# Kernel tuning notes

Hardware: AMD Instinct MI355X
Metric: run time of the kernel (lower is better)

The kernel has to match this reference:

```python
import jax, jax.numpy as jnp
import numpy as np

EPS = 1e-8


def setup_inputs() -> dict:
    key = jax.random.key(0)
    k1, k2, k3, k4, k5 = jax.random.split(key, 5)
    B, N_LOG, N_PHYS, E = 16, 512, 2048, 2048
    P = jax.random.uniform(k1, (B, N_LOG, N_PHYS), dtype=jnp.float32)
    d_hw = jax.random.randint(k2, (N_PHYS, N_PHYS), 0, 4, dtype=jnp.int32)
    edge_src = jax.random.randint(k3, (B, E), 0, N_LOG, dtype=jnp.int32)
    edge_dst = jax.random.randint(k4, (B, E), 0, N_LOG, dtype=jnp.int32)
    edge_w = jax.random.uniform(k5, (B, E), dtype=jnp.float32)
    return {"P": P, "d_hw": d_hw, "edge_src": edge_src,
            "edge_dst": edge_dst, "edge_w": edge_w}


def reference(P, d_hw, edge_src, edge_dst, edge_w):
    # A_hw[p,q] = 1 where hardware distance == 1 (adjacent qubits)
    A_hw = (d_hw == 1).astype(P.dtype)                      # [Q, Q]
    B = P.shape[0]
    # Dense contraction once per batch: PA[b,i,q] = sum_p P[b,i,p] A[p,q]
    PA = jnp.einsum('bip,pq->biq', P, A_hw)                 # [B, N, Q]
    b_idx = jnp.arange(B)[:, None]                          # [B, 1]
    gi = PA[b_idx, edge_src]                                # [B, E, Q]
    gj = P[b_idx, edge_dst]                                 # [B, E, Q]
    adj_score = jnp.einsum('beq,beq->be', gi, gj)           # [B, E]
    sample_adj = jnp.sum(edge_w * adj_score, axis=-1)       # [B]
    sample_weight = jnp.maximum(jnp.sum(edge_w, axis=-1), EPS)
    # every sample has edges -> valid_samples = B
    loss = -jnp.mean(sample_adj / sample_weight)
    return loss
```

## Files before the change

### kernel.cpp

```cpp
#include <hip/hip_runtime.h>
#include <hip/hip_bf16.h>

#define BATCH 16
#define NLOG 512
#define Q 2048
#define NEDGE 2048
#define M_TOT (BATCH * NLOG)
#define KB 2048
#define EDOT_BLOCKS 256

typedef float f32x2 __attribute__((ext_vector_type(2)));
typedef float f32x4 __attribute__((ext_vector_type(4)));
typedef int i32x4 __attribute__((ext_vector_type(4)));
typedef int i32x8 __attribute__((ext_vector_type(8)));

__device__ __forceinline__ unsigned char to_e4m3(float f) {
    int pk = __builtin_amdgcn_cvt_pk_fp8_f32(f, f, 0, false);
    return (unsigned char)(pk & 0xff);
}

__device__ __forceinline__ float dot16(i32x4 a, i32x4 b) {
    float s0 = 0.f, s1 = 0.f;
    #pragma unroll
    for (int d = 0; d < 4; d++) {
        f32x2 alo = __builtin_amdgcn_cvt_pk_f32_fp8(a[d], false);
        f32x2 ahi = __builtin_amdgcn_cvt_pk_f32_fp8(a[d], true);
        f32x2 blo = __builtin_amdgcn_cvt_pk_f32_fp8(b[d], false);
        f32x2 bhi = __builtin_amdgcn_cvt_pk_f32_fp8(b[d], true);
        s0 += alo[0] * blo[0] + alo[1] * blo[1];
        s1 += ahi[0] * bhi[0] + ahi[1] * bhi[1];
    }
    return s0 + s1;
}

__global__ __launch_bounds__(256) void prep(const float* __restrict__ P,
                                            unsigned char* __restrict__ P8,
                                            const int* __restrict__ d_hw,
                                            unsigned char* __restrict__ A8t,
                                            float* __restrict__ adj,
                                            float* __restrict__ wsum,
                                            unsigned* __restrict__ counter) {
    int bid = blockIdx.x;
    if (bid == 0) {
        if (threadIdx.x == 0) *counter = 0u;
        if (threadIdx.x < BATCH) { adj[threadIdx.x] = 0.f; wsum[threadIdx.x] = 0.f; }
    }
    if (bid < 8192) {
        int i = (bid * 256 + threadIdx.x) * 8;
        float4 v0 = *(const float4*)(P + i);
        float4 v1 = *(const float4*)(P + i + 4);
        int lo = 0, hi = 0;
        lo = __builtin_amdgcn_cvt_pk_fp8_f32(v0.x, v0.y, lo, false);
        lo = __builtin_amdgcn_cvt_pk_fp8_f32(v0.z, v0.w, lo, true);
        hi = __builtin_amdgcn_cvt_pk_fp8_f32(v1.x, v1.y, hi, false);
        hi = __builtin_amdgcn_cvt_pk_fp8_f32(v1.z, v1.w, hi, true);
        int2 st; st.x = lo; st.y = hi;
        *(int2*)(P8 + i) = st;
    } else {
        bid -= 8192;
        __shared__ unsigned char tile[32][33];
        int q0 = (bid & 63) * 32;
        int p0 = (bid >> 6) * 32;
        int tx = threadIdx.x & 31;
        int ty = threadIdx.x >> 5;
        for (int s = 0; s < 32; s += 8) {
            int p = p0 + ty + s;
            int v = d_hw[(size_t)p * Q + q0 + tx];
            tile[ty + s][tx] = (v == 1) ? 0x38 : 0x00;
        }
        __syncthreads();
        for (int s = 0; s < 32; s += 8) {
            A8t[(size_t)(q0 + ty + s) * Q + p0 + tx] = tile[tx][ty + s];
        }
    }
}

__global__ __launch_bounds__(256, 2) void gemm_bt8(const unsigned char* __restrict__ A,
                                                   const unsigned char* __restrict__ Bt,
                                                   unsigned char* __restrict__ PA8) {
    __shared__ unsigned char As[32768];
    __shared__ unsigned char Bs[16384];

    const int t = threadIdx.x;
    const int w = t >> 6;
    const int wr = w >> 1, wc = w & 1;
    const int l = t & 63;
    const int quad = l >> 4;
    const int lane16 = l & 15;

    const int m0 = blockIdx.x * 256;
    const int n0 = blockIdx.y * 128;

    const int s_row = t >> 3;
    const int s_off = (((t & 7) ^ (s_row & 7)) << 4);

    const int r7 = lane16 & 7;
    const int c0 = ((2 * quad) ^ r7) << 4;
    const int c1 = ((2 * quad + 1) ^ r7) << 4;

    f32x4 acc[8][4] = {};

    for (int k0 = 0; k0 < KB; k0 += 128) {
        #pragma unroll
        for (int c = 0; c < 8; c++) {
            const unsigned char* g = A + (size_t)(m0 + c * 32 + s_row) * KB + k0 + s_off;
            __builtin_amdgcn_global_load_lds(
                (const __attribute__((address_space(1))) void*)g,
                (__attribute__((address_space(3))) void*)(As + c * 4096 + w * 1024),
                16, 0, 0);
        }
        #pragma unroll
        for (int c = 0; c < 4; c++) {
            const unsigned char* g = Bt + (size_t)(n0 + c * 32 + s_row) * KB + k0 + s_off;
            __builtin_amdgcn_global_load_lds(
                (const __attribute__((address_space(1))) void*)g,
                (__attribute__((address_space(3))) void*)(Bs + c * 4096 + w * 1024),
                16, 0, 0);
        }
        __syncthreads();

        i32x8 bfr[4];
        #pragma unroll
        for (int j = 0; j < 4; j++) {
            int base = (wc * 64 + j * 16 + lane16) << 7;
            i32x4 lo = *(const i32x4*)(Bs + base + c0);
            i32x4 hi = *(const i32x4*)(Bs + base + c1);
            bfr[j] = __builtin_shufflevector(lo, hi, 0, 1, 2, 3, 4, 5, 6, 7);
        }
        #pragma unroll
        for (int i = 0; i < 8; i++) {
            int base = (wr * 128 + i * 16 + lane16) << 7;
            i32x4 lo = *(const i32x4*)(As + base + c0);
            i32x4 hi = *(const i32x4*)(As + base + c1);
            i32x8 af = __builtin_shufflevector(lo, hi, 0, 1, 2, 3, 4, 5, 6, 7);
            #pragma unroll
            for (int j = 0; j < 4; j++)
                acc[i][j] = __builtin_amdgcn_mfma_scale_f32_16x16x128_f8f6f4(
                    af, bfr[j], acc[i][j], 0, 0,
                    0, 127,
                    0, 127);
        }
        __syncthreads();
    }

    #pragma unroll
    for (int i = 0; i < 8; i++) {
        #pragma unroll
        for (int j = 0; j < 4; j++) {
            #pragma unroll
            for (int r = 0; r < 4; r++) {
                int row = m0 + wr * 128 + i * 16 + quad * 4 + r;
                int col = n0 + wc * 64 + j * 16 + lane16;
                PA8[(size_t)row * Q + col] = to_e4m3(acc[i][j][r] * (1.0f / 256.0f));
            }
        }
    }
}

__global__ __launch_bounds__(512) void edge_dot(const unsigned char* __restrict__ PA8,
                                                const unsigned char* __restrict__ P8,
                                                const int* __restrict__ esrc,
                                                const int* __restrict__ edst,
                                                const float* __restrict__ ew,
                                                float* __restrict__ adj,
                                                float* __restrict__ wsum,
                                                unsigned* __restrict__ counter,
                                                float* __restrict__ out) {
    const int lid = blockIdx.x;
    const int b = (lid & 7) | ((lid >> 7) << 3);
    const int chunk = (lid >> 3) & 15;
    const int t = threadIdx.x;
    const int w = t >> 6;
    const int lane = t & 63;

    const int e0 = b * NEDGE + chunk * 128 + w * 16;
    const unsigned char* Ab = PA8 + (size_t)b * NLOG * Q;
    const unsigned char* Bb = P8  + (size_t)b * NLOG * Q;
    const int off = lane * 32;

    int src = esrc[e0], dst = edst[e0];
    float wcur = ew[e0];
    const unsigned char* ap = Ab + (size_t)src * Q + off;
    const unsigned char* bp = Bb + (size_t)dst * Q + off;
    i32x4 A0 = *(const i32x4*)ap;
    i32x4 A1 = *(const i32x4*)(ap + 16);
    i32x4 B0 = *(const i32x4*)bp;
    i32x4 B1 = *(const i32x4*)(bp + 16);

    float acc = 0.f;
    float wacc = 0.f;
    #pragma unroll
    for (int e = 0; e < 16; e++) {
        i32x4 nA0 = A0, nA1 = A1, nB0 = B0, nB1 = B1;
        float wnext = 0.f;
        if (e < 15) {
            int ns = esrc[e0 + e + 1], nd = edst[e0 + e + 1];
            wnext = ew[e0 + e + 1];
            const unsigned char* nap = Ab + (size_t)ns * Q + off;
            const unsigned char* nbp = Bb + (size_t)nd * Q + off;
            nA0 = *(const i32x4*)nap;
            nA1 = *(const i32x4*)(nap + 16);
            nB0 = *(const i32x4*)nbp;
            nB1 = *(const i32x4*)(nbp + 16);
        }
        float p = dot16(A0, B0) + dot16(A1, B1);
        acc += wcur * p;
        wacc += wcur;
        A0 = nA0; A1 = nA1; B0 = nB0; B1 = nB1; wcur = wnext;
    }

    #pragma unroll
    for (int o = 32; o > 0; o >>= 1) acc += __shfl_xor(acc, o);

    __shared__ float ra[8], rw[8];
    if (lane == 0) { ra[w] = acc; rw[w] = wacc; }
    __syncthreads();

    if (t == 0) {
        float a = 0.f, ws = 0.f;
        #pragma unroll
        for (int i = 0; i < 8; i++) { a += ra[i]; ws += rw[i]; }
        atomicAdd(&adj[b],  a * 256.0f);
        atomicAdd(&wsum[b], ws);
        __threadfence();
        if (atomicAdd(counter, 1u) == EDOT_BLOCKS - 1) {
            __threadfence();
            float s = 0.f;
            #pragma unroll
            for (int bb = 0; bb < BATCH; bb++) {
                float av = atomicAdd(&adj[bb], 0.0f);
                float wv = atomicAdd(&wsum[bb], 0.0f);
                s += av / fmaxf(wv, 1e-8f);
            }
            out[0] = -s / (float)BATCH;
        }
    }
}

extern "C" void kernel_launch(void* const* d_in, const int* in_sizes, int n_in,
                              void* d_out, int out_size, void* d_ws, size_t ws_size,
                              hipStream_t stream) {
    const float* P    = (const float*)d_in[0];
    const int* d_hw   = (const int*)d_in[1];
    const int* esrc   = (const int*)d_in[2];
    const int* edst   = (const int*)d_in[3];
    const float* ew   = (const float*)d_in[4];
    float* out        = (float*)d_out;

    char* ws = (char*)d_ws;
    unsigned char* P8  = (unsigned char*)ws;
    unsigned char* A8t = (unsigned char*)(ws + 16777216);
    unsigned char* PA8 = (unsigned char*)(ws + 20971520);
    float* adj         = (float*)(ws + 37748736);
    float* wsum        = (float*)(ws + 37748736 + 64);
    unsigned* counter  = (unsigned*)(ws + 37748736 + 128);

    prep<<<8192 + 4096, 256, 0, stream>>>(P, P8, d_hw, A8t, adj, wsum, counter);
    gemm_bt8<<<dim3(M_TOT / 256, Q / 128), 256, 0, stream>>>(P8, A8t, PA8);
    edge_dot<<<EDOT_BLOCKS, 512, 0, stream>>>(PA8, P8, esrc, edst, ew, adj, wsum, counter, out);
}
```

Baseline: 167.5 us.

## Spread edge_dot over more blocks and move final reduction to separate kernel

After: 177.1 us. 1.06x slower.

```diff
diff --git a/kernel.cpp b/kernel.cpp
--- a/kernel.cpp
+++ b/kernel.cpp
@@ -7,7 +7,7 @@
 #define NEDGE 2048
 #define M_TOT (BATCH * NLOG)
 #define KB 2048
-#define EDOT_BLOCKS 256
+#define EDOT_BLOCKS 2048
 
 typedef float f32x2 __attribute__((ext_vector_type(2)));
 typedef float f32x4 __attribute__((ext_vector_type(4)));
@@ -157,84 +157,89 @@
     }
 }
 
-__global__ __launch_bounds__(512) void edge_dot(const unsigned char* __restrict__ PA8,
+__global__ __launch_bounds__(256) void edge_dot(const unsigned char* __restrict__ PA8,
                                                 const unsigned char* __restrict__ P8,
                                                 const int* __restrict__ esrc,
                                                 const int* __restrict__ edst,
                                                 const float* __restrict__ ew,
                                                 float* __restrict__ adj,
-                                                float* __restrict__ wsum,
-                                                unsigned* __restrict__ counter,
-                                                float* __restrict__ out) {
+                                                float* __restrict__ wsum) {
     const int lid = blockIdx.x;
-    const int b = (lid & 7) | ((lid >> 7) << 3);
-    const int chunk = (lid >> 3) & 15;
+    const int idx = lid >> 3;
+    const int b = (lid & 7) | ((idx >> 7) << 3);
+    const int chunk = idx & 127;
     const int t = threadIdx.x;
     const int w = t >> 6;
     const int lane = t & 63;
-
-    const int e0 = b * NEDGE + chunk * 128 + w * 16;
+    const int off = lane * 32;
+
+    const int e0 = b * NEDGE + chunk * 16 + w * 4;
     const unsigned char* Ab = PA8 + (size_t)b * NLOG * Q;
     const unsigned char* Bb = P8  + (size_t)b * NLOG * Q;
-    const int off = lane * 32;
-
-    int src = esrc[e0], dst = edst[e0];
-    float wcur = ew[e0];
-    const unsigned char* ap = Ab + (size_t)src * Q + off;
-    const unsigned char* bp = Bb + (size_t)dst * Q + off;
-    i32x4 A0 = *(const i32x4*)ap;
-    i32x4 A1 = *(const i32x4*)(ap + 16);
-    i32x4 B0 = *(const i32x4*)bp;
-    i32x4 B1 = *(const i32x4*)(bp + 16);
-
-    float acc = 0.f;
-    float wacc = 0.f;
-    #pragma unroll
-    for (int e = 0; e < 16; e++) {
-        i32x4 nA0 = A0, nA1 = A1, nB0 = B0, nB1 = B1;
-        float wnext = 0.f;
-        if (e < 15) {
-            int ns = esrc[e0 + e + 1], nd = edst[e0 + e + 1];
-            wnext = ew[e0 + e + 1];
-            const unsigned char* nap = Ab + (size_t)ns * Q + off;
-            const unsigned char* nbp = Bb + (size_t)nd * Q + off;
-            nA0 = *(const i32x4*)nap;
-            nA1 = *(const i32x4*)(nap + 16);
-            nB0 = *(const i32x4*)nbp;
-            nB1 = *(const i32x4*)(nbp + 16);
-        }
-        float p = dot16(A0, B0) + dot16(A1, B1);
-        acc += wcur * p;
-        wacc += wcur;
-        A0 = nA0; A1 = nA1; B0 = nB0; B1 = nB1; wcur = wnext;
-    }
+
+    int src0 = esrc[e0 + 0], dst0 = edst[e0 + 0];
+    int src1 = esrc[e0 + 1], dst1 = edst[e0 + 1];
+    int src2 = esrc[e0 + 2], dst2 = edst[e0 + 2];
+    int src3 = esrc[e0 + 3], dst3 = edst[e0 + 3];
+    float w0 = ew[e0 + 0], w1 = ew[e0 + 1], w2 = ew[e0 + 2], w3 = ew[e0 + 3];
+
+    const unsigned char* a0 = Ab + (size_t)src0 * Q + off;
+    const unsigned char* b0 = Bb + (size_t)dst0 * Q + off;
+    const unsigned char* a1 = Ab + (size_t)src1 * Q + off;
+    const unsigned char* b1 = Bb + (size_t)dst1 * Q + off;
+    const unsigned char* a2 = Ab + (size_t)src2 * Q + off;
+    const unsigned char* b2 = Bb + (size_t)dst2 * Q + off;
+    const unsigned char* a3 = Ab + (size_t)src3 * Q + off;
+    const unsigned char* b3 = Bb + (size_t)dst3 * Q + off;
+
+    i32x4 A00 = *(const i32x4*)a0;
+    i32x4 A01 = *(const i32x4*)(a0 + 16);
+    i32x4 B00 = *(const i32x4*)b0;
+    i32x4 B01 = *(const i32x4*)(b0 + 16);
+    i32x4 A10 = *(const i32x4*)a1;
+    i32x4 A11 = *(const i32x4*)(a1 + 16);
+    i32x4 B10 = *(const i32x4*)b1;
+    i32x4 B11 = *(const i32x4*)(b1 + 16);
+
+    float acc = w0 * (dot16(A00, B00) + dot16(A01, B01));
+
+    i32x4 A20 = *(const i32x4*)a2;
+    i32x4 A21 = *(const i32x4*)(a2 + 16);
+    i32x4 B20 = *(const i32x4*)b2;
+    i32x4 B21 = *(const i32x4*)(b2 + 16);
+
+    acc += w1 * (dot16(A10, B10) + dot16(A11, B11));
+
+    i32x4 A30 = *(const i32x4*)a3;
+    i32x4 A31 = *(const i32x4*)(a3 + 16);
+    i32x4 B30 = *(const i32x4*)b3;
+    i32x4 B31 = *(const i32x4*)(b3 + 16);
+
+    acc += w2 * (dot16(A20, B20) + dot16(A21, B21));
+    acc += w3 * (dot16(A30, B30) + dot16(A31, B31));
 
     #pragma unroll
     for (int o = 32; o > 0; o >>= 1) acc += __shfl_xor(acc, o);
-
-    __shared__ float ra[8], rw[8];
+    float wacc = w0 + w1 + w2 + w3;
+
+    __shared__ float ra[4], rw[4];
     if (lane == 0) { ra[w] = acc; rw[w] = wacc; }
     __syncthreads();
-
     if (t == 0) {
-        float a = 0.f, ws = 0.f;
-        #pragma unroll
-        for (int i = 0; i < 8; i++) { a += ra[i]; ws += rw[i]; }
-        atomicAdd(&adj[b],  a * 256.0f);
-        atomicAdd(&wsum[b], ws);
-        __threadfence();
-        if (atomicAdd(counter, 1u) == EDOT_BLOCKS - 1) {
-            __threadfence();
-            float s = 0.f;
-            #pragma unroll
-            for (int bb = 0; bb < BATCH; bb++) {
-                float av = atomicAdd(&adj[bb], 0.0f);
-                float wv = atomicAdd(&wsum[bb], 0.0f);
-                s += av / fmaxf(wv, 1e-8f);
-            }
-            out[0] = -s / (float)BATCH;
-        }
-    }
+        atomicAdd(&adj[b],  (ra[0] + ra[1] + ra[2] + ra[3]) * 256.0f);
+        atomicAdd(&wsum[b], rw[0] + rw[1] + rw[2] + rw[3]);
+    }
+}
+
+__global__ __launch_bounds__(64) void finalize(const float* __restrict__ adj,
+                                               const float* __restrict__ wsum,
+                                               float* __restrict__ out) {
+    const int lane = threadIdx.x;
+    float s = 0.f;
+    if (lane < BATCH) s = adj[lane] / fmaxf(wsum[lane], 1e-8f);
+    #pragma unroll
+    for (int o = 8; o > 0; o >>= 1) s += __shfl_xor(s, o);
+    if (lane == 0) out[0] = -s / (float)BATCH;
 }
 
 extern "C" void kernel_launch(void* const* d_in, const int* in_sizes, int n_in,
@@ -257,5 +262,6 @@
 
     prep<<<8192 + 4096, 256, 0, stream>>>(P, P8, d_hw, A8t, adj, wsum, counter);
     gemm_bt8<<<dim3(M_TOT / 256, Q / 128), 256, 0, stream>>>(P8, A8t, PA8);
-    edge_dot<<<EDOT_BLOCKS, 512, 0, stream>>>(PA8, P8, esrc, edst, ew, adj, wsum, counter, out);
-}
+    edge_dot<<<EDOT_BLOCKS, 256, 0, stream>>>(PA8, P8, esrc, edst, ew, adj, wsum);
+    finalize<<<1, 64, 0, stream>>>(adj, wsum, out);
+}
```

## Double-buffer LDS in fp8 GEMM and split tile across 8 waves

Applied to the files above, without the earlier changes.

New measurement: 175.2 us. +4.6%, slower.

```diff
diff --git a/kernel.cpp b/kernel.cpp
--- a/kernel.cpp
+++ b/kernel.cpp
@@ -75,15 +75,60 @@
     }
 }
 
-__global__ __launch_bounds__(256, 2) void gemm_bt8(const unsigned char* __restrict__ A,
+#define GSTAGE(bufAs, bufBs, kk0)                                              \
+    {                                                                          \
+        _Pragma("unroll")                                                      \
+        for (int c = 0; c < 4; c++) {                                          \
+            const unsigned char* g =                                           \
+                A + (size_t)(m0 + c * 64 + s_row) * KB + (kk0) + s_off;        \
+            __builtin_amdgcn_global_load_lds(                                  \
+                (const __attribute__((address_space(1))) void*)g,              \
+                (__attribute__((address_space(3))) void*)((bufAs) + c * 8192 + w * 1024), \
+                16, 0, 0);                                                     \
+        }                                                                      \
+        _Pragma("unroll")                                                      \
+        for (int c = 0; c < 2; c++) {                                          \
+            const unsigned char* g =                                           \
+                Bt + (size_t)(n0 + c * 64 + s_row) * KB + (kk0) + s_off;       \
+            __builtin_amdgcn_global_load_lds(                                  \
+                (const __attribute__((address_space(1))) void*)g,              \
+                (__attribute__((address_space(3))) void*)((bufBs) + c * 8192 + w * 1024), \
+                16, 0, 0);                                                     \
+        }                                                                      \
+    }
+
+#define GCOMPUTE(bufAs, bufBs)                                                 \
+    {                                                                          \
+        i32x8 bfr[2];                                                          \
+        _Pragma("unroll")                                                      \
+        for (int j = 0; j < 2; j++) {                                          \
+            int base = (wc * 32 + j * 16 + lane16) << 7;                       \
+            i32x4 lo = *(const i32x4*)((bufBs) + base + c0);                   \
+            i32x4 hi = *(const i32x4*)((bufBs) + base + c1);                   \
+            bfr[j] = __builtin_shufflevector(lo, hi, 0, 1, 2, 3, 4, 5, 6, 7);  \
+        }                                                                      \
+        _Pragma("unroll")                                                      \
+        for (int i = 0; i < 8; i++) {                                          \
+            int base = (wr * 128 + i * 16 + lane16) << 7;                      \
+            i32x4 lo = *(const i32x4*)((bufAs) + base + c0);                   \
+            i32x4 hi = *(const i32x4*)((bufAs) + base + c1);                   \
+            i32x8 af = __builtin_shufflevector(lo, hi, 0, 1, 2, 3, 4, 5, 6, 7);\
+            _Pragma("unroll")                                                  \
+            for (int j = 0; j < 2; j++)                                        \
+                acc[i][j] = __builtin_amdgcn_mfma_scale_f32_16x16x128_f8f6f4(  \
+                    af, bfr[j], acc[i][j], 0, 0, 0, 127, 0, 127);              \
+        }                                                                      \
+    }
+
+__global__ __launch_bounds__(512, 2) void gemm_bt8(const unsigned char* __restrict__ A,
                                                    const unsigned char* __restrict__ Bt,
                                                    unsigned char* __restrict__ PA8) {
-    __shared__ unsigned char As[32768];
-    __shared__ unsigned char Bs[16384];
+    __shared__ unsigned char As[2][32768];
+    __shared__ unsigned char Bs[2][16384];
 
     const int t = threadIdx.x;
     const int w = t >> 6;
-    const int wr = w >> 1, wc = w & 1;
+    const int wr = w >> 2, wc = w & 3;
     const int l = t & 63;
     const int quad = l >> 4;
     const int lane16 = l & 15;
@@ -98,59 +143,28 @@
     const int c0 = ((2 * quad) ^ r7) << 4;
     const int c1 = ((2 * quad + 1) ^ r7) << 4;
 
-    f32x4 acc[8][4] = {};
-
-    for (int k0 = 0; k0 < KB; k0 += 128) {
-        #pragma unroll
-        for (int c = 0; c < 8; c++) {
-            const unsigned char* g = A + (size_t)(m0 + c * 32 + s_row) * KB + k0 + s_off;
-            __builtin_amdgcn_global_load_lds(
-                (const __attribute__((address_space(1))) void*)g,
-                (__attribute__((address_space(3))) void*)(As + c * 4096 + w * 1024),
-                16, 0, 0);
-        }
-        #pragma unroll
-        for (int c = 0; c < 4; c++) {
-            const unsigned char* g = Bt + (size_t)(n0 + c * 32 + s_row) * KB + k0 + s_off;
-            __builtin_amdgcn_global_load_lds(
-                (const __attribute__((address_space(1))) void*)g,
-                (__attribute__((address_space(3))) void*)(Bs + c * 4096 + w * 1024),
-                16, 0, 0);
-        }
+    f32x4 acc[8][2] = {};
+
+    GSTAGE(As[0], Bs[0], 0);
+    __syncthreads();
+
+    #pragma unroll 2
+    for (int kk = 0; kk < 15; kk++) {
+        const int cur = kk & 1;
+        GSTAGE(As[cur ^ 1], Bs[cur ^ 1], (kk + 1) * 128);
+        GCOMPUTE(As[cur], Bs[cur]);
         __syncthreads();
-
-        i32x8 bfr[4];
-        #pragma unroll
-        for (int j = 0; j < 4; j++) {
-            int base = (wc * 64 + j * 16 + lane16) << 7;
-            i32x4 lo = *(const i32x4*)(Bs + base + c0);
-            i32x4 hi = *(const i32x4*)(Bs + base + c1);
-            bfr[j] = __builtin_shufflevector(lo, hi, 0, 1, 2, 3, 4, 5, 6, 7);
-        }
-        #pragma unroll
-        for (int i = 0; i < 8; i++) {
-            int base = (wr * 128 + i * 16 + lane16) << 7;
-            i32x4 lo = *(const i32x4*)(As + base + c0);
-            i32x4 hi = *(const i32x4*)(As + base + c1);
-            i32x8 af = __builtin_shufflevector(lo, hi, 0, 1, 2, 3, 4, 5, 6, 7);
-            #pragma unroll
-            for (int j = 0; j < 4; j++)
-                acc[i][j] = __builtin_amdgcn_mfma_scale_f32_16x16x128_f8f6f4(
-                    af, bfr[j], acc[i][j], 0, 0,
-                    0, 127,
-                    0, 127);
-        }
-        __syncthreads();
-    }
+    }
+    GCOMPUTE(As[1], Bs[1]);
 
     #pragma unroll
     for (int i = 0; i < 8; i++) {
         #pragma unroll
-        for (int j = 0; j < 4; j++) {
+        for (int j = 0; j < 2; j++) {
             #pragma unroll
             for (int r = 0; r < 4; r++) {
                 int row = m0 + wr * 128 + i * 16 + quad * 4 + r;
-                int col = n0 + wc * 64 + j * 16 + lane16;
+                int col = n0 + wc * 32 + j * 16 + lane16;
                 PA8[(size_t)row * Q + col] = to_e4m3(acc[i][j][r] * (1.0f / 256.0f));
             }
         }
@@ -256,6 +270,6 @@
     unsigned* counter  = (unsigned*)(ws + 37748736 + 128);
 
     prep<<<8192 + 4096, 256, 0, stream>>>(P, P8, d_hw, A8t, adj, wsum, counter);
-    gemm_bt8<<<dim3(M_TOT / 256, Q / 128), 256, 0, stream>>>(P8, A8t, PA8);
+    gemm_bt8<<<dim3(M_TOT / 256, Q / 128), 512, 0, stream>>>(P8, A8t, PA8);
     edge_dot<<<EDOT_BLOCKS, 512, 0, stream>>>(PA8, P8, esrc, edst, ew, adj, wsum, counter, out);
 }
```
